# Kernel optimization log

Hardware: AMD Instinct MI355X
Metric: run time of the kernel (lower is better)

The kernel has to match this reference:

```python
import jax, jax.numpy as jnp
import numpy as np

N, G, H = 500_000, 25_000, 256


def setup_inputs() -> dict:
    key = jax.random.key(0)
    ks = jax.random.split(key, 8)
    node = jax.random.normal(ks[0], (N, H), dtype=jnp.float32)
    super_node = jax.random.normal(ks[1], (G, H), dtype=jnp.float32)
    segment_ids = jnp.sort(jax.random.randint(ks[2], (N,), 0, G, dtype=jnp.int32))
    s = 0.05
    return {
        "node": node,
        "super_node": super_node,
        "segment_ids": segment_ids,
        "w_align": jax.random.normal(ks[3], (2 * H, 1), jnp.float32) * s,
        "b_align": jnp.zeros((1,), jnp.float32),
        "w_attend": jax.random.normal(ks[4], (H, H), jnp.float32) * s,
        "b_attend": jnp.zeros((H,), jnp.float32),
        "w_ih": jax.random.normal(ks[5], (H, 3 * H), jnp.float32) * s,
        "w_hh": jax.random.normal(ks[6], (H, 3 * H), jnp.float32) * s,
        "b_ih": jnp.zeros((3 * H,), jnp.float32),
        "b_hh": jnp.zeros((3 * H,), jnp.float32),
    }


def reference(node, super_node, segment_ids, w_align, b_align, w_attend,
              b_attend, w_ih, w_hh, b_ih, b_hh):
    g = super_node.shape[0]
    h = node.shape[1]
    # super_node = F.leaky_relu(super_node)
    s = jax.nn.leaky_relu(super_node)  # slope 0.01 (torch default)
    # cal_alignment(cat([node, broadcast_nodes(super)])) == node@Wn + (s@Ws)[seg]
    wn, ws = w_align[:h], w_align[h:]
    score = jax.nn.leaky_relu(node @ wn + (s @ ws)[segment_ids] + b_align)  # [N,1]
    # softmax_nodes: segment-wise stable softmax
    m = jax.ops.segment_max(score, segment_ids, num_segments=g)
    w = jnp.exp(score - m[segment_ids])
    denom = jax.ops.segment_sum(w, segment_ids, num_segments=g)
    attn = w / denom[segment_ids]  # [N,1]
    # attend (dropout=0, eval)
    hidden = node @ w_attend + b_attend  # [N,H]
    # sum_nodes weighted by attention, then ELU
    ctx = jax.nn.elu(jax.ops.segment_sum(attn * hidden, segment_ids, num_segments=g))  # [G,H]
    # GRUCell(ctx, s) per torch semantics
    gi = ctx @ w_ih + b_ih
    gh = s @ w_hh + b_hh
    ir, iz, inn = jnp.split(gi, 3, axis=-1)
    hr, hz, hn = jnp.split(gh, 3, axis=-1)
    r = jax.nn.sigmoid(ir + hr)
    z = jax.nn.sigmoid(iz + hz)
    n = jnp.tanh(inn + r * hn)
    new_h = (1.0 - z) * n + z * s
    return jax.nn.relu(new_h), attn
```

## Files before the change

kernel.cpp:

```cpp
#include <hip/hip_runtime.h>
#include <math.h>

#define N_NODES 500000
#define G_SEG   25000
#define H_DIM   256
#define SPB     4

typedef __attribute__((ext_vector_type(4))) float f32x4;
typedef __attribute__((ext_vector_type(8))) short bf16x8;

__device__ __forceinline__ float leaky(float x){ return x > 0.f ? x : 0.01f * x; }

__device__ __forceinline__ ushort f2bf(float f){
  unsigned u = __float_as_uint(f);
  u += 0x7FFFu + ((u >> 16) & 1u);
  return (ushort)(u >> 16);
}

__global__ __launch_bounds__(256) void k_starts(
    const int* __restrict__ seg, int* __restrict__ starts)
{
  int i = blockIdx.x * 256 + threadIdx.x;
  if (i >= N_NODES) return;
  int s = seg[i];
  int prev = (i == 0) ? -1 : seg[i - 1];
  for (int g = prev + 1; g <= s; g++) starts[g] = i;
  if (i == N_NODES - 1)
    for (int g = s + 1; g <= G_SEG; g++) starts[g] = N_NODES;
}

__global__ __launch_bounds__(256) void kPack(
    const float* __restrict__ w_att, const float* __restrict__ w_ih,
    const float* __restrict__ w_hh, ushort* __restrict__ Bp,
    ushort* __restrict__ Bp6)
{
  int b = blockIdx.x, c = threadIdx.x;
  if (b < 256) {
    int kk = b;
    Bp[(((kk >> 3) << 8) + c) * 8 + (kk & 7)] = f2bf(w_att[kk * H_DIM + c]);
  } else {
    int kk = b - 256;
    #pragma unroll
    for (int gate = 0; gate < 4; gate++) {
      float v;
      if (gate == 0)      v = (kk < 256) ? w_ih[kk * 768 + c]        : w_hh[(kk - 256) * 768 + c];
      else if (gate == 1) v = (kk < 256) ? w_ih[kk * 768 + 256 + c]  : w_hh[(kk - 256) * 768 + 256 + c];
      else if (gate == 2) v = (kk < 256) ? w_ih[kk * 768 + 512 + c]  : 0.f;
      else                v = (kk < 256) ? 0.f                       : w_hh[(kk - 256) * 768 + 512 + c];
      int n = (gate << 8) + c;
      Bp6[(((kk >> 3) << 10) + n) * 8 + (kk & 7)] = f2bf(v);
    }
  }
}

__global__ __launch_bounds__(256) void k1_prep_super(
    const float* __restrict__ sn, const float* __restrict__ w_align,
    float* __restrict__ s_buf, float* __restrict__ sws)
{
  int g = blockIdx.x, t = threadIdx.x;
  float v = sn[g * H_DIM + t];
  float sv = leaky(v);
  s_buf[g * H_DIM + t] = sv;
  float p = sv * w_align[H_DIM + t];
  #pragma unroll
  for (int d = 1; d < 64; d <<= 1) p += __shfl_xor(p, d);
  __shared__ float red[4];
  int wid = t >> 6, lane = t & 63;
  if (lane == 0) red[wid] = p;
  __syncthreads();
  if (t == 0) sws[g] = red[0] + red[1] + red[2] + red[3];
}

__global__ __launch_bounds__(256) void kF_score_softmax_agg(
    const float* __restrict__ node, const int* __restrict__ starts,
    const float* __restrict__ w_align, const float* __restrict__ b_align,
    const float* __restrict__ sws,
    float* __restrict__ attn_out, float* __restrict__ agg,
    float* __restrict__ bscale)
{
  __shared__ float cpart[4][H_DIM];
  __shared__ float wm[4], wsum[4];
  __shared__ int st_s[SPB + 1];

  const int tid = threadIdx.x;
  const int g0 = blockIdx.x * SPB;
  if (tid <= SPB) st_s[tid] = starts[g0 + tid];
  __syncthreads();

  const int wv = tid >> 6, lane = tid & 63;
  const float4 wvec = ((const float4*)w_align)[lane];
  const float b0 = b_align[0];

  for (int j = 0; j < SPB; j++) {
    const int g = g0 + j;
    const int st = st_s[j], en = st_s[j + 1];
    const float swsg = sws[g];

    float m = -3.4e38f, sum = 0.f;
    f32x4 pacc = {0.f, 0.f, 0.f, 0.f};

    int r = st + wv;
    for (; r + 12 < en; r += 16) {
      f32x4 a0 = ((const f32x4*)node)[(size_t)(r     ) * 64 + lane];
      f32x4 a1 = ((const f32x4*)node)[(size_t)(r +  4) * 64 + lane];
      f32x4 a2 = ((const f32x4*)node)[(size_t)(r +  8) * 64 + lane];
      f32x4 a3 = ((const f32x4*)node)[(size_t)(r + 12) * 64 + lane];
      float d0 = a0[0]*wvec.x + a0[1]*wvec.y + a0[2]*wvec.z + a0[3]*wvec.w;
      float d1 = a1[0]*wvec.x + a1[1]*wvec.y + a1[2]*wvec.z + a1[3]*wvec.w;
      float d2 = a2[0]*wvec.x + a2[1]*wvec.y + a2[2]*wvec.z + a2[3]*wvec.w;
      float d3 = a3[0]*wvec.x + a3[1]*wvec.y + a3[2]*wvec.z + a3[3]*wvec.w;
      #pragma unroll
      for (int s2 = 1; s2 < 64; s2 <<= 1) {
        d0 += __shfl_xor(d0, s2);
        d1 += __shfl_xor(d1, s2);
        d2 += __shfl_xor(d2, s2);
        d3 += __shfl_xor(d3, s2);
      }
      float sc0 = leaky(d0 + swsg + b0);
      float sc1 = leaky(d1 + swsg + b0);
      float sc2 = leaky(d2 + swsg + b0);
      float sc3 = leaky(d3 + swsg + b0);
      if (lane == 0) {
        attn_out[r] = sc0; attn_out[r + 4] = sc1;
        attn_out[r + 8] = sc2; attn_out[r + 12] = sc3;
      }
      float bm = fmaxf(fmaxf(sc0, sc1), fmaxf(sc2, sc3));
      if (bm > m) {
        float scale = __expf(m - bm);
        sum *= scale; pacc *= scale; m = bm;
      }
      float p0 = __expf(sc0 - m), p1 = __expf(sc1 - m);
      float p2 = __expf(sc2 - m), p3 = __expf(sc3 - m);
      sum += (p0 + p1) + (p2 + p3);
      pacc += p0 * a0 + p1 * a1;
      pacc += p2 * a2 + p3 * a3;
    }
    for (; r < en; r += 4) {
      f32x4 a = ((const f32x4*)node)[(size_t)r * 64 + lane];
      float d = a[0]*wvec.x + a[1]*wvec.y + a[2]*wvec.z + a[3]*wvec.w;
      #pragma unroll
      for (int s2 = 1; s2 < 64; s2 <<= 1) d += __shfl_xor(d, s2);
      float sc = leaky(d + swsg + b0);
      if (lane == 0) attn_out[r] = sc;
      if (sc <= m) {
        float p = __expf(sc - m);
        sum += p;
        pacc += p * a;
      } else {
        float scale = __expf(m - sc);
        sum = sum * scale + 1.f;
        pacc = pacc * scale + a;
        m = sc;
      }
    }

    if (j > 0) __syncthreads();
    ((f32x4*)&cpart[wv][0])[lane] = pacc;
    if (lane == 0) { wm[wv] = m; wsum[wv] = sum; }
    __syncthreads();

    float m0 = fmaxf(fmaxf(wm[0], wm[1]), fmaxf(wm[2], wm[3]));
    float f0 = (wm[0] > -1e38f) ? __expf(wm[0] - m0) : 0.f;
    float f1 = (wm[1] > -1e38f) ? __expf(wm[1] - m0) : 0.f;
    float f2 = (wm[2] > -1e38f) ? __expf(wm[2] - m0) : 0.f;
    float f3 = (wm[3] > -1e38f) ? __expf(wm[3] - m0) : 0.f;
    float D = wsum[0] * f0 + wsum[1] * f1 + wsum[2] * f2 + wsum[3] * f3;
    float invD = (D > 0.f) ? 1.f / D : 0.f;

    float v = cpart[0][tid] * f0 + cpart[1][tid] * f1 +
              cpart[2][tid] * f2 + cpart[3][tid] * f3;
    agg[(size_t)g * H_DIM + tid] = v * invD;
    if (tid == 0) bscale[g] = (D > 0.f) ? 1.f : 0.f;

    for (int rr = st + tid; rr < en; rr += 256)
      attn_out[rr] = __expf(attn_out[rr] - m0) * invD;
  }
}

__global__ __launch_bounds__(256, 2) void k5b_ctx(
    const float* __restrict__ agg, const ushort* __restrict__ Bp,
    const float* __restrict__ b_att, const float* __restrict__ bscale,
    float* __restrict__ ctx)
{
  __shared__ __align__(16) ushort A_lds[128 * 256];

  const int tid  = threadIdx.x;
  const int row0 = blockIdx.x * 128;

  #pragma unroll
  for (int i = 0; i < 16; i++) {
    int v = tid + i * 256;
    int r = v >> 5;
    int s = v & 31;
    int grow = row0 + r;
    f32x4 x0 = {0.f, 0.f, 0.f, 0.f}, x1 = {0.f, 0.f, 0.f, 0.f};
    if (grow < G_SEG) {
      const f32x4* p = (const f32x4*)(agg + (size_t)grow * H_DIM) + s * 2;
      x0 = p[0]; x1 = p[1];
    }
    bf16x8 t;
    t[0] = (short)f2bf(x0[0]); t[1] = (short)f2bf(x0[1]);
    t[2] = (short)f2bf(x0[2]); t[3] = (short)f2bf(x0[3]);
    t[4] = (short)f2bf(x1[0]); t[5] = (short)f2bf(x1[1]);
    t[6] = (short)f2bf(x1[2]); t[7] = (short)f2bf(x1[3]);
    *(bf16x8*)&A_lds[r * 256 + ((s ^ (r & 7)) * 8)] = t;
  }
  __syncthreads();

  const int wv  = tid >> 6;
  const int l   = tid & 63;
  const int l15 = l & 15, lq = l >> 4, l7 = l & 7;
  const int colbase = wv * 64 + l15;

  f32x4 acc[8][4];
  #pragma unroll
  for (int mf = 0; mf < 8; mf++)
    #pragma unroll
    for (int nf = 0; nf < 4; nf++)
      acc[mf][nf] = (f32x4){0.f, 0.f, 0.f, 0.f};

  for (int ks = 0; ks < 8; ks++) {
    int c = ks * 4 + lq;
    bf16x8 b[4];
    #pragma unroll
    for (int nf = 0; nf < 4; nf++)
      b[nf] = *(const bf16x8*)&Bp[(((c << 8) + colbase + nf * 16)) * 8];
    bf16x8 a[8];
    #pragma unroll
    for (int mf = 0; mf < 8; mf++)
      a[mf] = *(const bf16x8*)&A_lds[(mf * 16 + l15) * 256 + ((c ^ l7) * 8)];
    #pragma unroll
    for (int mf = 0; mf < 8; mf++)
      #pragma unroll
      for (int nf = 0; nf < 4; nf++)
        acc[mf][nf] = __builtin_amdgcn_mfma_f32_16x16x32_bf16(
            a[mf], b[nf], acc[mf][nf], 0, 0, 0);
  }

  float bias[4];
  #pragma unroll
  for (int nf = 0; nf < 4; nf++) bias[nf] = b_att[colbase + nf * 16];

  #pragma unroll
  for (int mf = 0; mf < 8; mf++) {
    #pragma unroll
    for (int r = 0; r < 4; r++) {
      int grow = row0 + mf * 16 + lq * 4 + r;
      if (grow < G_SEG) {
        float bsc = bscale[grow];
        #pragma unroll
        for (int nf = 0; nf < 4; nf++)
          ctx[(size_t)grow * H_DIM + colbase + nf * 16] =
              acc[mf][nf][r] + bias[nf] * bsc;
      }
    }
  }
}

__global__ __launch_bounds__(256, 2) void k6_mfma(
    const float* __restrict__ ctxbuf, const float* __restrict__ s_buf,
    const ushort* __restrict__ Bp6,
    const float* __restrict__ b_ih, const float* __restrict__ b_hh,
    float* __restrict__ out0)
{
  __shared__ __align__(16) ushort A_lds[32 * 512];

  const int tid  = threadIdx.x;
  const int row0 = blockIdx.x * 32;

  #pragma unroll
  for (int i = 0; i < 8; i++) {
    int v = tid + i * 256;
    int r = v >> 6;
    int s = v & 63;
    int g = row0 + r;
    f32x4 x0 = {0.f, 0.f, 0.f, 0.f}, x1 = {0.f, 0.f, 0.f, 0.f};
    if (g < G_SEG) {
      const f32x4* p = (s < 32)
          ? (const f32x4*)(ctxbuf + (size_t)g * H_DIM) + s * 2
          : (const f32x4*)(s_buf + (size_t)g * H_DIM) + (s - 32) * 2;
      x0 = p[0]; x1 = p[1];
      if (s < 32) {
        #pragma unroll
        for (int e = 0; e < 4; e++) {
          x0[e] = x0[e] > 0.f ? x0[e] : (__expf(x0[e]) - 1.f);
          x1[e] = x1[e] > 0.f ? x1[e] : (__expf(x1[e]) - 1.f);
        }
      }
    }
    bf16x8 t;
    t[0] = (short)f2bf(x0[0]); t[1] = (short)f2bf(x0[1]);
    t[2] = (short)f2bf(x0[2]); t[3] = (short)f2bf(x0[3]);
    t[4] = (short)f2bf(x1[0]); t[5] = (short)f2bf(x1[1]);
    t[6] = (short)f2bf(x1[2]); t[7] = (short)f2bf(x1[3]);
    *(bf16x8*)&A_lds[r * 512 + ((s ^ (r & 7)) * 8)] = t;
  }
  __syncthreads();

  const int wv  = tid >> 6;
  const int l   = tid & 63;
  const int l15 = l & 15, lq = l >> 4, l7 = l & 7;

  f32x4 acc[4][2][4];
  #pragma unroll
  for (int gt = 0; gt < 4; gt++)
    #pragma unroll
    for (int mf = 0; mf < 2; mf++)
      #pragma unroll
      for (int nf = 0; nf < 4; nf++)
        acc[gt][mf][nf] = (f32x4){0.f, 0.f, 0.f, 0.f};

  for (int ks = 0; ks < 16; ks++) {
    int c = ks * 4 + lq;
    bf16x8 a[2];
    #pragma unroll
    for (int mf = 0; mf < 2; mf++)
      a[mf] = *(const bf16x8*)&A_lds[(mf * 16 + l15) * 512 + ((c ^ l7) * 8)];
    #pragma unroll
    for (int gt = 0; gt < 4; gt++) {
      if (gt == 2 && ks >= 8) continue;
      if (gt == 3 && ks < 8) continue;
      #pragma unroll
      for (int nf = 0; nf < 4; nf++) {
        int n = (gt << 8) + (wv << 6) + nf * 16 + l15;
        bf16x8 b = *(const bf16x8*)&Bp6[(((c << 10) + n)) * 8];
        acc[gt][0][nf] = __builtin_amdgcn_mfma_f32_16x16x32_bf16(
            a[0], b, acc[gt][0][nf], 0, 0, 0);
        acc[gt][1][nf] = __builtin_amdgcn_mfma_f32_16x16x32_bf16(
            a[1], b, acc[gt][1][nf], 0, 0, 0);
      }
    }
  }

  #pragma unroll
  for (int nf = 0; nf < 4; nf++) {
    int cc = (wv << 6) + nf * 16 + l15;
    float bir = b_ih[cc] + b_hh[cc];
    float biz = b_ih[256 + cc] + b_hh[256 + cc];
    float bin_ = b_ih[512 + cc];
    float bhn  = b_hh[512 + cc];
    #pragma unroll
    for (int mf = 0; mf < 2; mf++) {
      #pragma unroll
      for (int rr = 0; rr < 4; rr++) {
        int grow = row0 + mf * 16 + lq * 4 + rr;
        if (grow < G_SEG) {
          float v0 = acc[0][mf][nf][rr];
          float v1 = acc[1][mf][nf][rr];
          float v2 = acc[2][mf][nf][rr];
          float v3 = acc[3][mf][nf][rr];
          float r_ = 1.f / (1.f + __expf(-(v0 + bir)));
          float z_ = 1.f / (1.f + __expf(-(v1 + biz)));
          float n_ = tanhf(v2 + bin_ + r_ * (v3 + bhn));
          float sv = s_buf[(size_t)grow * H_DIM + cc];
          float nh = (1.f - z_) * n_ + z_ * sv;
          out0[(size_t)grow * H_DIM + cc] = nh > 0.f ? nh : 0.f;
        }
      }
    }
  }
}

extern "C" void kernel_launch(void* const* d_in, const int* in_sizes, int n_in,
                              void* d_out, int out_size, void* d_ws, size_t ws_size,
                              hipStream_t stream)
{
  (void)in_sizes; (void)n_in; (void)out_size; (void)ws_size;
  const float* node       = (const float*)d_in[0];
  const float* super_node = (const float*)d_in[1];
  const int*   seg        = (const int*)d_in[2];
  const float* w_align    = (const float*)d_in[3];
  const float* b_align    = (const float*)d_in[4];
  const float* w_att      = (const float*)d_in[5];
  const float* b_att      = (const float*)d_in[6];
  const float* w_ih       = (const float*)d_in[7];
  const float* w_hh       = (const float*)d_in[8];
  const float* b_ih       = (const float*)d_in[9];
  const float* b_hh       = (const float*)d_in[10];

  float* out0     = (float*)d_out;
  float* attn_out = (float*)d_out + (size_t)G_SEG * H_DIM;

  float* ws     = (float*)d_ws;
  float* s_buf  = ws;
  float* sws    = ws + 6400000;
  float* agg    = ws + 6425000;
  ushort* Bp    = (ushort*)(ws + 12825000);
  ushort* Bp6   = (ushort*)(ws + 12860000);
  float* bscale = ws + 13125000;
  int*   starts = (int*)(ws + 13150000);
  float* ctx    = ws + 13200000;

  k_starts<<<(N_NODES + 255) / 256, 256, 0, stream>>>(seg, starts);
  kPack<<<768, 256, 0, stream>>>(w_att, w_ih, w_hh, Bp, Bp6);
  k1_prep_super<<<G_SEG, 256, 0, stream>>>(super_node, w_align, s_buf, sws);
  kF_score_softmax_agg<<<G_SEG / SPB, 256, 0, stream>>>(
      node, starts, w_align, b_align, sws, attn_out, agg, bscale);
  k5b_ctx<<<(G_SEG + 127) / 128, 256, 0, stream>>>(agg, Bp, b_att, bscale, ctx);
  k6_mfma<<<(G_SEG + 31) / 32, 256, 0, stream>>>(ctx, s_buf, Bp6, b_ih, b_hh, out0);
}
```

Measured before the change: 277.6 us.

## Assign one wavefront per segment in score-softmax-aggregate kernel

The fused score/softmax/aggregation kernel changes from four wavefronts cooperating on each segment, one segment at a time, to each wavefront handling its own segment. This removes the shared-memory partial merge and the block-wide barriers that were needed per segment, and the attention normalization becomes wave-local. The cost is load imbalance, since segments of different sizes now run in parallel waves of one block. Each wave also has less memory-level parallelism, because the unrolled loop now walks consecutive rows of a single segment.

```diff
diff --git a/kernel.cpp b/kernel.cpp
--- a/kernel.cpp
+++ b/kernel.cpp
@@ -78,10 +78,7 @@
     float* __restrict__ attn_out, float* __restrict__ agg,
     float* __restrict__ bscale)
 {
-  __shared__ float cpart[4][H_DIM];
-  __shared__ float wm[4], wsum[4];
   __shared__ int st_s[SPB + 1];
-
   const int tid = threadIdx.x;
   const int g0 = blockIdx.x * SPB;
   if (tid <= SPB) st_s[tid] = starts[g0 + tid];
@@ -91,90 +88,73 @@
   const float4 wvec = ((const float4*)w_align)[lane];
   const float b0 = b_align[0];
 
-  for (int j = 0; j < SPB; j++) {
-    const int g = g0 + j;
-    const int st = st_s[j], en = st_s[j + 1];
-    const float swsg = sws[g];
-
-    float m = -3.4e38f, sum = 0.f;
-    f32x4 pacc = {0.f, 0.f, 0.f, 0.f};
-
-    int r = st + wv;
-    for (; r + 12 < en; r += 16) {
-      f32x4 a0 = ((const f32x4*)node)[(size_t)(r     ) * 64 + lane];
-      f32x4 a1 = ((const f32x4*)node)[(size_t)(r +  4) * 64 + lane];
-      f32x4 a2 = ((const f32x4*)node)[(size_t)(r +  8) * 64 + lane];
-      f32x4 a3 = ((const f32x4*)node)[(size_t)(r + 12) * 64 + lane];
-      float d0 = a0[0]*wvec.x + a0[1]*wvec.y + a0[2]*wvec.z + a0[3]*wvec.w;
-      float d1 = a1[0]*wvec.x + a1[1]*wvec.y + a1[2]*wvec.z + a1[3]*wvec.w;
-      float d2 = a2[0]*wvec.x + a2[1]*wvec.y + a2[2]*wvec.z + a2[3]*wvec.w;
-      float d3 = a3[0]*wvec.x + a3[1]*wvec.y + a3[2]*wvec.z + a3[3]*wvec.w;
-      #pragma unroll
-      for (int s2 = 1; s2 < 64; s2 <<= 1) {
-        d0 += __shfl_xor(d0, s2);
-        d1 += __shfl_xor(d1, s2);
-        d2 += __shfl_xor(d2, s2);
-        d3 += __shfl_xor(d3, s2);
-      }
-      float sc0 = leaky(d0 + swsg + b0);
-      float sc1 = leaky(d1 + swsg + b0);
-      float sc2 = leaky(d2 + swsg + b0);
-      float sc3 = leaky(d3 + swsg + b0);
-      if (lane == 0) {
-        attn_out[r] = sc0; attn_out[r + 4] = sc1;
-        attn_out[r + 8] = sc2; attn_out[r + 12] = sc3;
-      }
-      float bm = fmaxf(fmaxf(sc0, sc1), fmaxf(sc2, sc3));
-      if (bm > m) {
-        float scale = __expf(m - bm);
-        sum *= scale; pacc *= scale; m = bm;
-      }
-      float p0 = __expf(sc0 - m), p1 = __expf(sc1 - m);
-      float p2 = __expf(sc2 - m), p3 = __expf(sc3 - m);
-      sum += (p0 + p1) + (p2 + p3);
-      pacc += p0 * a0 + p1 * a1;
-      pacc += p2 * a2 + p3 * a3;
-    }
-    for (; r < en; r += 4) {
-      f32x4 a = ((const f32x4*)node)[(size_t)r * 64 + lane];
-      float d = a[0]*wvec.x + a[1]*wvec.y + a[2]*wvec.z + a[3]*wvec.w;
-      #pragma unroll
-      for (int s2 = 1; s2 < 64; s2 <<= 1) d += __shfl_xor(d, s2);
-      float sc = leaky(d + swsg + b0);
-      if (lane == 0) attn_out[r] = sc;
-      if (sc <= m) {
-        float p = __expf(sc - m);
-        sum += p;
-        pacc += p * a;
-      } else {
-        float scale = __expf(m - sc);
-        sum = sum * scale + 1.f;
-        pacc = pacc * scale + a;
-        m = sc;
-      }
-    }
-
-    if (j > 0) __syncthreads();
-    ((f32x4*)&cpart[wv][0])[lane] = pacc;
-    if (lane == 0) { wm[wv] = m; wsum[wv] = sum; }
-    __syncthreads();
-
-    float m0 = fmaxf(fmaxf(wm[0], wm[1]), fmaxf(wm[2], wm[3]));
-    float f0 = (wm[0] > -1e38f) ? __expf(wm[0] - m0) : 0.f;
-    float f1 = (wm[1] > -1e38f) ? __expf(wm[1] - m0) : 0.f;
-    float f2 = (wm[2] > -1e38f) ? __expf(wm[2] - m0) : 0.f;
-    float f3 = (wm[3] > -1e38f) ? __expf(wm[3] - m0) : 0.f;
-    float D = wsum[0] * f0 + wsum[1] * f1 + wsum[2] * f2 + wsum[3] * f3;
-    float invD = (D > 0.f) ? 1.f / D : 0.f;
-
-    float v = cpart[0][tid] * f0 + cpart[1][tid] * f1 +
-              cpart[2][tid] * f2 + cpart[3][tid] * f3;
-    agg[(size_t)g * H_DIM + tid] = v * invD;
-    if (tid == 0) bscale[g] = (D > 0.f) ? 1.f : 0.f;
-
-    for (int rr = st + tid; rr < en; rr += 256)
-      attn_out[rr] = __expf(attn_out[rr] - m0) * invD;
-  }
+  const int g  = g0 + wv;
+  const int st = st_s[wv], en = st_s[wv + 1];
+  const float swsg = sws[g];
+
+  float m = -3.4e38f, sum = 0.f;
+  f32x4 pacc = {0.f, 0.f, 0.f, 0.f};
+
+  int r = st;
+  for (; r + 3 < en; r += 4) {
+    f32x4 a0 = ((const f32x4*)node)[(size_t)(r    ) * 64 + lane];
+    f32x4 a1 = ((const f32x4*)node)[(size_t)(r + 1) * 64 + lane];
+    f32x4 a2 = ((const f32x4*)node)[(size_t)(r + 2) * 64 + lane];
+    f32x4 a3 = ((const f32x4*)node)[(size_t)(r + 3) * 64 + lane];
+    float d0 = a0[0]*wvec.x + a0[1]*wvec.y + a0[2]*wvec.z + a0[3]*wvec.w;
+    float d1 = a1[0]*wvec.x + a1[1]*wvec.y + a1[2]*wvec.z + a1[3]*wvec.w;
+    float d2 = a2[0]*wvec.x + a2[1]*wvec.y + a2[2]*wvec.z + a2[3]*wvec.w;
+    float d3 = a3[0]*wvec.x + a3[1]*wvec.y + a3[2]*wvec.z + a3[3]*wvec.w;
+    #pragma unroll
+    for (int s2 = 1; s2 < 64; s2 <<= 1) {
+      d0 += __shfl_xor(d0, s2);
+      d1 += __shfl_xor(d1, s2);
+      d2 += __shfl_xor(d2, s2);
+      d3 += __shfl_xor(d3, s2);
+    }
+    float sc0 = leaky(d0 + swsg + b0);
+    float sc1 = leaky(d1 + swsg + b0);
+    float sc2 = leaky(d2 + swsg + b0);
+    float sc3 = leaky(d3 + swsg + b0);
+    if (lane < 4) {
+      float scs = (lane == 0) ? sc0 : (lane == 1) ? sc1 : (lane == 2) ? sc2 : sc3;
+      attn_out[r + lane] = scs;
+    }
+    float bm = fmaxf(fmaxf(sc0, sc1), fmaxf(sc2, sc3));
+    if (bm > m) {
+      float scale = __expf(m - bm);
+      sum *= scale; pacc *= scale; m = bm;
+    }
+    float p0 = __expf(sc0 - m), p1 = __expf(sc1 - m);
+    float p2 = __expf(sc2 - m), p3 = __expf(sc3 - m);
+    sum += (p0 + p1) + (p2 + p3);
+    pacc += p0 * a0 + p1 * a1;
+    pacc += p2 * a2 + p3 * a3;
+  }
+  for (; r < en; r++) {
+    f32x4 a = ((const f32x4*)node)[(size_t)r * 64 + lane];
+    float d = a[0]*wvec.x + a[1]*wvec.y + a[2]*wvec.z + a[3]*wvec.w;
+    #pragma unroll
+    for (int s2 = 1; s2 < 64; s2 <<= 1) d += __shfl_xor(d, s2);
+    float sc = leaky(d + swsg + b0);
+    if (lane == 0) attn_out[r] = sc;
+    if (sc <= m) {
+      float p = __expf(sc - m);
+      sum += p;
+      pacc += p * a;
+    } else {
+      float scale = __expf(m - sc);
+      sum = sum * scale + 1.f;
+      pacc = pacc * scale + a;
+      m = sc;
+    }
+  }
+
+  float invD = (sum > 0.f) ? 1.f / sum : 0.f;
+  ((f32x4*)(agg + (size_t)g * H_DIM))[lane] = pacc * invD;
+  if (lane == 0) bscale[g] = (sum > 0.f) ? 1.f : 0.f;
+  for (int rr = st + lane; rr < en; rr += 64)
+    attn_out[rr] = __expf(attn_out[rr] - m) * invD;
 }
 
 __global__ __launch_bounds__(256, 2) void k5b_ctx(
```

After: 270.4 us. -2.6%, faster.
